# Performance work log

Hardware: AMD Instinct MI355X
Metric: run time of the kernel (lower is better)

The kernel has to match this reference:

```python
import jax, jax.numpy as jnp
import numpy as np
import math

EMBED_DIM = 1024
NUM_HEADS = 16
HEAD_DIM = EMBED_DIM // NUM_HEADS          # 64
SUB_HEAD_DIM = HEAD_DIM // 2               # 32
SCALING = 1.0 / math.sqrt(SUB_HEAD_DIM)
LAMBDA_INIT = 0.8 - 0.6 * math.exp(-0.3 * 0)  # layer_idx = 0 -> 0.2


def setup_inputs() -> dict:
    key = jax.random.key(0)
    ks = jax.random.split(key, 10)
    B, T, D = 2, 2048, EMBED_DIM
    xav = math.sqrt(6.0 / (D + D))  # xavier_uniform bound for square-ish mats
    return {
        "query": jax.random.normal(ks[0], (B, T, D), jnp.float32),
        "key": jax.random.normal(ks[1], (B, T, D), jnp.float32),
        "value": jax.random.normal(ks[2], (B, T, D), jnp.float32),
        "in_proj_weight": jax.random.uniform(ks[3], (3 * D, D), jnp.float32, -xav, xav),
        "in_proj_bias": jnp.zeros((3 * D,), jnp.float32),
        "out_proj_weight": jax.random.uniform(ks[4], (D, D), jnp.float32, -xav, xav),
        "out_proj_bias": jnp.zeros((D,), jnp.float32),
        "lambda_q1": 0.1 * jax.random.normal(ks[5], (SUB_HEAD_DIM,), jnp.float32),
        "lambda_k1": 0.1 * jax.random.normal(ks[6], (SUB_HEAD_DIM,), jnp.float32),
        "lambda_q2": 0.1 * jax.random.normal(ks[7], (SUB_HEAD_DIM,), jnp.float32),
        "lambda_k2": 0.1 * jax.random.normal(ks[8], (SUB_HEAD_DIM,), jnp.float32),
    }


def reference(query, key, value, in_proj_weight, in_proj_bias,
              out_proj_weight, out_proj_bias,
              lambda_q1, lambda_k1, lambda_q2, lambda_k2):
    B, T, D = query.shape
    S = key.shape[1]
    H, hd, sd = NUM_HEADS, HEAD_DIM, SUB_HEAD_DIM

    qw, kw, vw = jnp.split(in_proj_weight, 3, axis=0)
    qb, kb, vb = jnp.split(in_proj_bias, 3, axis=0)
    q = query @ qw.T + qb
    k = key @ kw.T + kb
    v = value @ vw.T + vb

    # [B, H, T, head_dim]
    q = q.reshape(B, T, H, hd).transpose(0, 2, 1, 3)
    k = k.reshape(B, S, H, hd).transpose(0, 2, 1, 3)
    v = v.reshape(B, S, H, hd).transpose(0, 2, 1, 3)

    q1, q2 = q[..., :sd], q[..., sd:]
    k1, k2 = k[..., :sd], k[..., sd:]

    logits_1 = jnp.einsum('bhtd,bhsd->bhts', q1, k1) * SCALING
    logits_2 = jnp.einsum('bhtd,bhsd->bhts', q2, k2) * SCALING

    a1 = jax.nn.softmax(logits_1, axis=-1)
    a2 = jax.nn.softmax(logits_2, axis=-1)

    lam = (jnp.exp(jnp.dot(lambda_q1, lambda_k1))
           - jnp.exp(jnp.dot(lambda_q2, lambda_k2)) + LAMBDA_INIT)

    diff_weights = a1 - lam * a2
    attn_output = jnp.einsum('bhts,bhsd->bhtd', diff_weights, v)
    attn_output = attn_output * (1.0 - LAMBDA_INIT)

    attn_output = attn_output.transpose(0, 2, 1, 3).reshape(B, T, D)
    output = attn_output @ out_proj_weight.T + out_proj_bias
    return output
```

## Files before the change

kernel.cpp:

```cpp
#include <hip/hip_runtime.h>
#include <cstdint>
#include <cstddef>

typedef unsigned short u16;
typedef __attribute__((ext_vector_type(8))) short bf16x8;
typedef __attribute__((ext_vector_type(4))) short bf16x4;
typedef __attribute__((ext_vector_type(4))) float f32x4;

__device__ __forceinline__ u16 f2bf(float f) {
  uint32_t u = __float_as_uint(f);
  u += 0x7fffu + ((u >> 16) & 1u);
  return (u16)(u >> 16);
}

__device__ __forceinline__ short f2bfs(float f) {
  __bf16 h = (__bf16)f;
  return __builtin_bit_cast(short, h);
}

__device__ __forceinline__ float bf2f(u16 u) {
  return __uint_as_float(((uint32_t)u) << 16);
}

#define MFMA16(a, b, c) __builtin_amdgcn_mfma_f32_16x16x32_bf16((a), (b), (c), 0, 0, 0)

__device__ __forceinline__ float ex2(float x) {
#if __has_builtin(__builtin_amdgcn_exp2f)
  return __builtin_amdgcn_exp2f(x);
#else
  return exp2f(x);
#endif
}

__global__ __launch_bounds__(256) void cvt_kernel(const float* __restrict__ in,
                                                  u16* __restrict__ out, int n8) {
  int i = blockIdx.x * blockDim.x + threadIdx.x;
  if (i >= n8) return;
  const float4* p = (const float4*)in;
  float4 a = p[i * 2], b = p[i * 2 + 1];
  u16 o[8] = {f2bf(a.x), f2bf(a.y), f2bf(a.z), f2bf(a.w),
              f2bf(b.x), f2bf(b.y), f2bf(b.z), f2bf(b.w)};
  *(int4*)(out + (size_t)i * 8) = *(const int4*)o;
}

template <typename OUT_T, bool SPLIT_A>
__global__ __launch_bounds__(256) void gemm_bt(const u16* __restrict__ Abase,
                                               const u16* __restrict__ B,
                                               const float* __restrict__ bias,
                                               OUT_T* __restrict__ C,
                                               u16* __restrict__ QH, u16* __restrict__ KH,
                                               u16* __restrict__ VT,
                                               int M, int N, int K) {
  __shared__ u16 As[128][40];
  __shared__ u16 Bs[128][40];
  const int nb = blockIdx.x, mb = blockIdx.y;
  const int t = threadIdx.x;
  const u16* A = Abase + (SPLIT_A ? (size_t)(nb >> 3) * (size_t)M * K : (size_t)0);
  const int w = t >> 6, lane = t & 63;
  const int wr = w >> 1, wc = w & 1;
  const int lr = lane & 15, lk = lane >> 4;
  const f32x4 zero4 = {0.f, 0.f, 0.f, 0.f};
  f32x4 acc[4][4];
#pragma unroll
  for (int i = 0; i < 4; ++i)
#pragma unroll
    for (int j = 0; j < 4; ++j) acc[i][j] = zero4;

  const int srow = t >> 2;
  const int scol = (t & 3) << 3;
  const u16* Ap = A + (size_t)(mb * 128 + srow) * K + scol;
  const u16* Bp = B + (size_t)(nb * 128 + srow) * K + scol;

  for (int k0 = 0; k0 < K; k0 += 32) {
    __syncthreads();
    *(int4*)&As[srow][scol]      = *(const int4*)(Ap + k0);
    *(int4*)&As[srow + 64][scol] = *(const int4*)(Ap + (size_t)64 * K + k0);
    *(int4*)&Bs[srow][scol]      = *(const int4*)(Bp + k0);
    *(int4*)&Bs[srow + 64][scol] = *(const int4*)(Bp + (size_t)64 * K + k0);
    __syncthreads();
    bf16x8 af[4], bfr[4];
#pragma unroll
    for (int mf = 0; mf < 4; ++mf) af[mf] = *(const bf16x8*)&As[wr * 64 + mf * 16 + lr][lk * 8];
#pragma unroll
    for (int nf = 0; nf < 4; ++nf) bfr[nf] = *(const bf16x8*)&Bs[wc * 64 + nf * 16 + lr][lk * 8];
#pragma unroll
    for (int mf = 0; mf < 4; ++mf)
#pragma unroll
      for (int nf = 0; nf < 4; ++nf) acc[mf][nf] = MFMA16(af[mf], bfr[nf], acc[mf][nf]);
  }

  if constexpr (SPLIT_A) {
    const int third = nb >> 3;
    const int bb = mb >> 4;
#pragma unroll
    for (int nf = 0; nf < 4; ++nf) {
      const int col = nb * 128 + wc * 64 + nf * 16 + lr;
      const int c = col & 1023;
      const int h = c >> 6, d = c & 63;
      const float bv = bias[col];
      u16* qk = (third == 0 ? QH : KH) + (size_t)(bb * 16 + h) * 2048 * 64;
      u16* vt = VT + ((size_t)(bb * 16 + h) * 64 + d) * 2048;
#pragma unroll
      for (int mf = 0; mf < 4; ++mf) {
        const int row0 = mb * 128 + wr * 64 + mf * 16 + lk * 4;
        const int s0 = row0 & 2047;
        if (third < 2) {
#pragma unroll
          for (int r = 0; r < 4; ++r)
            qk[(size_t)(s0 + r) * 64 + d] = f2bf(acc[mf][nf][r] + bv);
        } else {
          u16 tmp[4];
#pragma unroll
          for (int r = 0; r < 4; ++r) tmp[r] = f2bf(acc[mf][nf][r] + bv);
          *(uint2*)&vt[s0] = *(const uint2*)tmp;
        }
      }
    }
  } else {
#pragma unroll
    for (int nf = 0; nf < 4; ++nf) {
      const int col = nb * 128 + wc * 64 + nf * 16 + lr;
      const float bv = bias[col];
#pragma unroll
      for (int mf = 0; mf < 4; ++mf) {
        const int row0 = mb * 128 + wr * 64 + mf * 16 + lk * 4;
#pragma unroll
        for (int r = 0; r < 4; ++r)
          ((float*)C)[(size_t)(row0 + r) * N + col] = acc[mf][nf][r] + bv;
      }
    }
  }
}

__global__ __launch_bounds__(256, 4) void diff_attn(const u16* __restrict__ QH,
                                                    const u16* __restrict__ KH,
                                                    const u16* __restrict__ VT,
                                                    const float* __restrict__ lq1,
                                                    const float* __restrict__ lk1,
                                                    const float* __restrict__ lq2,
                                                    const float* __restrict__ lk2,
                                                    u16* __restrict__ ATTN) {
  __shared__ u16 Ks[64][68];
  __shared__ u16 Vs[64][68];
  const int t = threadIdx.x;
  const int id = blockIdx.x;
  const int swz = (id & 7) * 128 + (id >> 3);
  const int qt = swz & 31, bh = swz >> 5;
  const int b = bh >> 4, h = bh & 15;
  const int w = t >> 6, lane = t & 63;
  const int lr = lane & 15, lk = lane >> 4;
  const float QSC = 0.17677669529663687f * 1.4426950408889634f;

  float dd1 = 0.f, dd2 = 0.f;
  for (int i = 0; i < 32; ++i) { dd1 += lq1[i] * lk1[i]; dd2 += lq2[i] * lk2[i]; }
  const float lam = __expf(dd1) - __expf(dd2) + 0.2f;

  const int srow = t >> 3;
  const int scol = (t & 7) << 3;
  const int krow = ((srow & 4) << 2) | ((srow & 24) >> 1) | (srow & 3);
  const u16* qh = QH + (size_t)(b * 16 + h) * 2048 * 64;
  const u16* kh = KH + (size_t)(b * 16 + h) * 2048 * 64;
  const u16* vt = VT + (size_t)(b * 16 + h) * 64 * 2048;

  bf16x8 qa[2];
#pragma unroll
  for (int hh = 0; hh < 2; ++hh) {
    bf16x8 q = *(const bf16x8*)(qh + (size_t)(qt * 64 + w * 16 + lr) * 64 + hh * 32 + lk * 8);
#pragma unroll
    for (int i = 0; i < 8; ++i) q[i] = f2bfs(bf2f((u16)q[i]) * QSC);
    qa[hh] = q;
  }

  const f32x4 zero4 = {0.f, 0.f, 0.f, 0.f};
  f32x4 O[2][4], Ol[2];
#pragma unroll
  for (int hh = 0; hh < 2; ++hh) {
    Ol[hh] = zero4;
#pragma unroll
    for (int df = 0; df < 4; ++df) O[hh][df] = zero4;
  }
  bf16x8 vone8;
#pragma unroll
  for (int i = 0; i < 8; ++i) vone8[i] = (short)0x3F80;

  const u16* kp0 = kh + (size_t)srow * 64 + scol;
  const u16* kp1 = kp0 + (size_t)32 * 64;
  const u16* vp0 = vt + (size_t)srow * 2048 + scol;
  const u16* vp1 = vp0 + (size_t)32 * 2048;

  int4 kA0 = *(const int4*)kp0;
  int4 kA1 = *(const int4*)kp1;
  int4 vA0 = *(const int4*)vp0;
  int4 vA1 = *(const int4*)vp1;
  int4 kB0, kB1, vB0, vB1;

  for (int it = 0; it < 32; ++it) {
    __syncthreads();
    *(int4*)&Ks[krow][scol]      = kA0;
    *(int4*)&Ks[krow + 32][scol] = kA1;
    *(int4*)&Vs[srow][scol]      = vA0;
    *(int4*)&Vs[srow + 32][scol] = vA1;
    if (it < 31) {
      const int s1 = (it + 1) * 64;
      kB0 = *(const int4*)(kp0 + (size_t)s1 * 64);
      kB1 = *(const int4*)(kp1 + (size_t)s1 * 64);
      vB0 = *(const int4*)(vp0 + s1);
      vB1 = *(const int4*)(vp1 + s1);
    }
    __syncthreads();

    bf16x8 pk8[2][2];
#pragma unroll
    for (int hh = 0; hh < 2; ++hh) {
      f32x4 St[4];
#pragma unroll
      for (int nf = 0; nf < 4; ++nf) {
        bf16x8 kb = *(const bf16x8*)&Ks[nf * 16 + lr][hh * 32 + lk * 8];
        St[nf] = MFMA16(kb, qa[hh], zero4);
      }
#pragma unroll
      for (int j = 0; j < 2; ++j) {
        bf16x8 p;
#pragma unroll
        for (int a = 0; a < 2; ++a)
#pragma unroll
          for (int r = 0; r < 4; ++r)
            p[a * 4 + r] = f2bfs(ex2(St[2 * j + a][r]));
        pk8[hh][j] = p;
      }
    }

    __builtin_amdgcn_s_setprio(1);
#pragma unroll
    for (int j = 0; j < 2; ++j) {
      const bf16x8 pa0 = pk8[0][j], pa1 = pk8[1][j];
#pragma unroll
      for (int df = 0; df < 4; ++df) {
        bf16x8 vb = *(const bf16x8*)&Vs[df * 16 + lr][j * 32 + lk * 8];
        O[0][df] = MFMA16(pa0, vb, O[0][df]);
        O[1][df] = MFMA16(pa1, vb, O[1][df]);
      }
      Ol[0] = MFMA16(pa0, vone8, Ol[0]);
      Ol[1] = MFMA16(pa1, vone8, Ol[1]);
    }
    __builtin_amdgcn_s_setprio(0);

    kA0 = kB0; kA1 = kB1; vA0 = vB0; vA1 = vB1;
  }

  float i1[4], i2[4];
#pragma unroll
  for (int r = 0; r < 4; ++r) {
    i1[r] = 1.f / Ol[0][r];
    i2[r] = 1.f / Ol[1][r];
  }
  const size_t qrow0 = (size_t)b * 2048 + (size_t)qt * 64;
#pragma unroll
  for (int df = 0; df < 4; ++df) {
    const int col = h * 64 + df * 16 + lr;
#pragma unroll
    for (int r = 0; r < 4; ++r) {
      const size_t row = qrow0 + w * 16 + lk * 4 + r;
      float v = 0.8f * (O[0][df][r] * i1[r] - lam * O[1][df][r] * i2[r]);
      ATTN[row * 1024 + col] = f2bf(v);
    }
  }
}

extern "C" void kernel_launch(void* const* d_in, const int* in_sizes, int n_in,
                              void* d_out, int out_size, void* d_ws, size_t ws_size,
                              hipStream_t stream) {
  (void)in_sizes; (void)n_in; (void)out_size; (void)ws_size;
  const float* query = (const float*)d_in[0];
  const float* key_  = (const float*)d_in[1];
  const float* value = (const float*)d_in[2];
  const float* ipw   = (const float*)d_in[3];
  const float* ipb   = (const float*)d_in[4];
  const float* opw   = (const float*)d_in[5];
  const float* opb   = (const float*)d_in[6];
  const float* lq1   = (const float*)d_in[7];
  const float* lk1   = (const float*)d_in[8];
  const float* lq2   = (const float*)d_in[9];
  const float* lk2   = (const float*)d_in[10];

  const int M = 4096, D = 1024;
  u16* X    = (u16*)d_ws;
  u16* Wqkv = X + (size_t)3 * M * D;
  u16* Wout = Wqkv + (size_t)3 * D * D;
  u16* QH   = Wout + (size_t)D * D;
  u16* KH   = QH + (size_t)M * D;
  u16* VT   = KH + (size_t)M * D;
  u16* ATTN = VT + (size_t)M * D;

  auto cvt = [&](const float* src, u16* dst, size_t n) {
    int n8 = (int)(n / 8);
    cvt_kernel<<<dim3((n8 + 255) / 256), dim3(256), 0, stream>>>(src, dst, n8);
  };
  cvt(query, X, (size_t)M * D);
  cvt(key_,  X + (size_t)M * D, (size_t)M * D);
  cvt(value, X + (size_t)2 * M * D, (size_t)M * D);
  cvt(ipw, Wqkv, (size_t)3 * D * D);
  cvt(opw, Wout, (size_t)D * D);

  gemm_bt<u16, true><<<dim3(24, 32), dim3(256), 0, stream>>>(
      X, Wqkv, ipb, (u16*)nullptr, QH, KH, VT, M, 3 * D, D);
  diff_attn<<<dim3(1024), dim3(256), 0, stream>>>(QH, KH, VT, lq1, lk1, lq2, lk2, ATTN);
  gemm_bt<float, false><<<dim3(8, 32), dim3(256), 0, stream>>>(
      ATTN, Wout, opb, (float*)d_out, nullptr, nullptr, nullptr, M, D, D);
}
```

Before: 159.6 us.

## Double KV tile per attention iteration and batch fp32-to-bf16 conversion launches

The attention kernel now stages 128 keys and values per loop iteration instead of 64, halving the number of block-wide barriers and prefetch rounds, and processes the tile in two 64-key sub-steps. Shared memory per block roughly doubles, which may reduce how many blocks fit per CU under the 4-block launch bound, and more registers are spent on prefetch buffers. The five separate conversion launches are also merged into two kernels using the grid y dimension, cutting launch overhead.

New measurement: 412.0 us. 2.58x slower.

```diff
diff --git a/kernel.cpp b/kernel.cpp
--- a/kernel.cpp
+++ b/kernel.cpp
@@ -32,15 +32,41 @@
 #endif
 }
 
-__global__ __launch_bounds__(256) void cvt_kernel(const float* __restrict__ in,
-                                                  u16* __restrict__ out, int n8) {
+__global__ __launch_bounds__(256) void cvt3_kernel(const float* __restrict__ q,
+                                                   const float* __restrict__ k,
+                                                   const float* __restrict__ v,
+                                                   u16* __restrict__ out, int n8) {
   int i = blockIdx.x * blockDim.x + threadIdx.x;
   if (i >= n8) return;
-  const float4* p = (const float4*)in;
+  const float* src = blockIdx.y == 0 ? q : (blockIdx.y == 1 ? k : v);
+  u16* dst = out + (size_t)blockIdx.y * n8 * 8;
+  const float4* p = (const float4*)src;
   float4 a = p[i * 2], b = p[i * 2 + 1];
   u16 o[8] = {f2bf(a.x), f2bf(a.y), f2bf(a.z), f2bf(a.w),
               f2bf(b.x), f2bf(b.y), f2bf(b.z), f2bf(b.w)};
-  *(int4*)(out + (size_t)i * 8) = *(const int4*)o;
+  *(int4*)(dst + (size_t)i * 8) = *(const int4*)o;
+}
+
+__global__ __launch_bounds__(256) void cvtw_kernel(const float* __restrict__ w0,
+                                                   const float* __restrict__ w1,
+                                                   u16* __restrict__ o0,
+                                                   u16* __restrict__ o1,
+                                                   int n8_0, int n8_1) {
+  int i = blockIdx.x * blockDim.x + threadIdx.x;
+  const float* src;
+  u16* dst;
+  if (blockIdx.y == 0) {
+    if (i >= n8_0) return;
+    src = w0; dst = o0;
+  } else {
+    if (i >= n8_1) return;
+    src = w1; dst = o1;
+  }
+  const float4* p = (const float4*)src;
+  float4 a = p[i * 2], b = p[i * 2 + 1];
+  u16 o[8] = {f2bf(a.x), f2bf(a.y), f2bf(a.z), f2bf(a.w),
+              f2bf(b.x), f2bf(b.y), f2bf(b.z), f2bf(b.w)};
+  *(int4*)(dst + (size_t)i * 8) = *(const int4*)o;
 }
 
 template <typename OUT_T, bool SPLIT_A>
@@ -140,8 +166,8 @@
                                                     const float* __restrict__ lq2,
                                                     const float* __restrict__ lk2,
                                                     u16* __restrict__ ATTN) {
-  __shared__ u16 Ks[64][68];
-  __shared__ u16 Vs[64][68];
+  __shared__ u16 Ks[128][68];
+  __shared__ u16 Vs[64][136];
   const int t = threadIdx.x;
   const int id = blockIdx.x;
   const int swz = (id & 7) * 128 + (id >> 3);
@@ -183,69 +209,79 @@
 #pragma unroll
   for (int i = 0; i < 8; ++i) vone8[i] = (short)0x3F80;
 
-  const u16* kp0 = kh + (size_t)srow * 64 + scol;
-  const u16* kp1 = kp0 + (size_t)32 * 64;
-  const u16* vp0 = vt + (size_t)srow * 2048 + scol;
-  const u16* vp1 = vp0 + (size_t)32 * 2048;
-
-  int4 kA0 = *(const int4*)kp0;
-  int4 kA1 = *(const int4*)kp1;
-  int4 vA0 = *(const int4*)vp0;
-  int4 vA1 = *(const int4*)vp1;
-  int4 kB0, kB1, vB0, vB1;
-
-  for (int it = 0; it < 32; ++it) {
+  const u16* kp = kh + (size_t)srow * 64 + scol;
+  const u16* vp = vt + (size_t)srow * 2048 + scol;
+
+  int4 kA[4], vA[4], kB[4], vB[4];
+#pragma unroll
+  for (int kk = 0; kk < 4; ++kk) kA[kk] = *(const int4*)(kp + (size_t)(kk * 32) * 64);
+  vA[0] = *(const int4*)vp;
+  vA[1] = *(const int4*)(vp + 64);
+  vA[2] = *(const int4*)(vp + (size_t)32 * 2048);
+  vA[3] = *(const int4*)(vp + (size_t)32 * 2048 + 64);
+
+  for (int it = 0; it < 16; ++it) {
     __syncthreads();
-    *(int4*)&Ks[krow][scol]      = kA0;
-    *(int4*)&Ks[krow + 32][scol] = kA1;
-    *(int4*)&Vs[srow][scol]      = vA0;
-    *(int4*)&Vs[srow + 32][scol] = vA1;
-    if (it < 31) {
-      const int s1 = (it + 1) * 64;
-      kB0 = *(const int4*)(kp0 + (size_t)s1 * 64);
-      kB1 = *(const int4*)(kp1 + (size_t)s1 * 64);
-      vB0 = *(const int4*)(vp0 + s1);
-      vB1 = *(const int4*)(vp1 + s1);
+#pragma unroll
+    for (int kk = 0; kk < 4; ++kk)
+      *(int4*)&Ks[kk * 32 + krow][scol] = kA[kk];
+    *(int4*)&Vs[srow][scol]            = vA[0];
+    *(int4*)&Vs[srow][64 + scol]       = vA[1];
+    *(int4*)&Vs[srow + 32][scol]       = vA[2];
+    *(int4*)&Vs[srow + 32][64 + scol]  = vA[3];
+    if (it < 15) {
+      const int s1 = (it + 1) * 128;
+#pragma unroll
+      for (int kk = 0; kk < 4; ++kk)
+        kB[kk] = *(const int4*)(kp + (size_t)(s1 + kk * 32) * 64);
+      vB[0] = *(const int4*)(vp + s1);
+      vB[1] = *(const int4*)(vp + s1 + 64);
+      vB[2] = *(const int4*)(vp + (size_t)32 * 2048 + s1);
+      vB[3] = *(const int4*)(vp + (size_t)32 * 2048 + s1 + 64);
     }
     __syncthreads();
 
-    bf16x8 pk8[2][2];
-#pragma unroll
-    for (int hh = 0; hh < 2; ++hh) {
-      f32x4 St[4];
-#pragma unroll
-      for (int nf = 0; nf < 4; ++nf) {
-        bf16x8 kb = *(const bf16x8*)&Ks[nf * 16 + lr][hh * 32 + lk * 8];
-        St[nf] = MFMA16(kb, qa[hh], zero4);
+#pragma unroll
+    for (int sub = 0; sub < 2; ++sub) {
+      bf16x8 pk8[2][2];
+#pragma unroll
+      for (int hh = 0; hh < 2; ++hh) {
+        f32x4 St[4];
+#pragma unroll
+        for (int nf = 0; nf < 4; ++nf) {
+          bf16x8 kb = *(const bf16x8*)&Ks[sub * 64 + nf * 16 + lr][hh * 32 + lk * 8];
+          St[nf] = MFMA16(kb, qa[hh], zero4);
+        }
+#pragma unroll
+        for (int j = 0; j < 2; ++j) {
+          bf16x8 p;
+#pragma unroll
+          for (int a = 0; a < 2; ++a)
+#pragma unroll
+            for (int r = 0; r < 4; ++r)
+              p[a * 4 + r] = f2bfs(ex2(St[2 * j + a][r]));
+          pk8[hh][j] = p;
+        }
       }
+
+      __builtin_amdgcn_s_setprio(1);
 #pragma unroll
       for (int j = 0; j < 2; ++j) {
-        bf16x8 p;
-#pragma unroll
-        for (int a = 0; a < 2; ++a)
-#pragma unroll
-          for (int r = 0; r < 4; ++r)
-            p[a * 4 + r] = f2bfs(ex2(St[2 * j + a][r]));
-        pk8[hh][j] = p;
+        const bf16x8 pa0 = pk8[0][j], pa1 = pk8[1][j];
+#pragma unroll
+        for (int df = 0; df < 4; ++df) {
+          bf16x8 vb = *(const bf16x8*)&Vs[df * 16 + lr][sub * 64 + j * 32 + lk * 8];
+          O[0][df] = MFMA16(pa0, vb, O[0][df]);
+          O[1][df] = MFMA16(pa1, vb, O[1][df]);
+        }
+        Ol[0] = MFMA16(pa0, vone8, Ol[0]);
+        Ol[1] = MFMA16(pa1, vone8, Ol[1]);
       }
-    }
-
-    __builtin_amdgcn_s_setprio(1);
-#pragma unroll
-    for (int j = 0; j < 2; ++j) {
-      const bf16x8 pa0 = pk8[0][j], pa1 = pk8[1][j];
-#pragma unroll
-      for (int df = 0; df < 4; ++df) {
-        bf16x8 vb = *(const bf16x8*)&Vs[df * 16 + lr][j * 32 + lk * 8];
-        O[0][df] = MFMA16(pa0, vb, O[0][df]);
-        O[1][df] = MFMA16(pa1, vb, O[1][df]);
-      }
-      Ol[0] = MFMA16(pa0, vone8, Ol[0]);
-      Ol[1] = MFMA16(pa1, vone8, Ol[1]);
-    }
-    __builtin_amdgcn_s_setprio(0);
-
-    kA0 = kB0; kA1 = kB1; vA0 = vB0; vA1 = vB1;
+      __builtin_amdgcn_s_setprio(0);
+    }
+
+#pragma unroll
+    for (int kk = 0; kk < 4; ++kk) { kA[kk] = kB[kk]; vA[kk] = vB[kk]; }
   }
 
   float i1[4], i2[4];
@@ -292,15 +328,17 @@
   u16* VT   = KH + (size_t)M * D;
   u16* ATTN = VT + (size_t)M * D;
 
-  auto cvt = [&](const float* src, u16* dst, size_t n) {
-    int n8 = (int)(n / 8);
-    cvt_kernel<<<dim3((n8 + 255) / 256), dim3(256), 0, stream>>>(src, dst, n8);
-  };
-  cvt(query, X, (size_t)M * D);
-  cvt(key_,  X + (size_t)M * D, (size_t)M * D);
-  cvt(value, X + (size_t)2 * M * D, (size_t)M * D);
-  cvt(ipw, Wqkv, (size_t)3 * D * D);
-  cvt(opw, Wout, (size_t)D * D);
+  {
+    int n8 = (int)((size_t)M * D / 8);
+    cvt3_kernel<<<dim3((n8 + 255) / 256, 3), dim3(256), 0, stream>>>(
+        query, key_, value, X, n8);
+  }
+  {
+    int n8_0 = (int)((size_t)3 * D * D / 8);
+    int n8_1 = (int)((size_t)D * D / 8);
+    cvtw_kernel<<<dim3((n8_0 + 255) / 256, 2), dim3(256), 0, stream>>>(
+        ipw, opw, Wqkv, Wout, n8_0, n8_1);
+  }
 
   gemm_bt<u16, true><<<dim3(24, 32), dim3(256), 0, stream>>>(
       X, Wqkv, ipb, (u16*)nullptr, QH, KH, VT, M, 3 * D, D);
```

## Merge conversion launches and double GEMM K-tile to 64

Applied to the files above, without the earlier changes.

Five fp32-to-bf16 conversion launches are merged into two kernels that use a 2D grid, cutting launch overhead. The GEMM K-step is doubled from 32 to 64 and the LDS tiles are widened with padding to 68, halving the number of barrier-separated load/compute iterations. This uses more LDS per block, which may lower occupancy, and the new padding changes the bank-conflict pattern.

After: 145.8 us. 8.6% less time.

```diff
diff --git a/kernel.cpp b/kernel.cpp
--- a/kernel.cpp
+++ b/kernel.cpp
@@ -32,15 +32,41 @@
 #endif
 }
 
-__global__ __launch_bounds__(256) void cvt_kernel(const float* __restrict__ in,
-                                                  u16* __restrict__ out, int n8) {
+__global__ __launch_bounds__(256) void cvt3_kernel(const float* __restrict__ q,
+                                                   const float* __restrict__ k,
+                                                   const float* __restrict__ v,
+                                                   u16* __restrict__ out, int n8) {
   int i = blockIdx.x * blockDim.x + threadIdx.x;
   if (i >= n8) return;
-  const float4* p = (const float4*)in;
+  const float* src = blockIdx.y == 0 ? q : (blockIdx.y == 1 ? k : v);
+  u16* dst = out + (size_t)blockIdx.y * n8 * 8;
+  const float4* p = (const float4*)src;
   float4 a = p[i * 2], b = p[i * 2 + 1];
   u16 o[8] = {f2bf(a.x), f2bf(a.y), f2bf(a.z), f2bf(a.w),
               f2bf(b.x), f2bf(b.y), f2bf(b.z), f2bf(b.w)};
-  *(int4*)(out + (size_t)i * 8) = *(const int4*)o;
+  *(int4*)(dst + (size_t)i * 8) = *(const int4*)o;
+}
+
+__global__ __launch_bounds__(256) void cvtw_kernel(const float* __restrict__ w0,
+                                                   const float* __restrict__ w1,
+                                                   u16* __restrict__ o0,
+                                                   u16* __restrict__ o1,
+                                                   int n8_0, int n8_1) {
+  int i = blockIdx.x * blockDim.x + threadIdx.x;
+  const float* src;
+  u16* dst;
+  if (blockIdx.y == 0) {
+    if (i >= n8_0) return;
+    src = w0; dst = o0;
+  } else {
+    if (i >= n8_1) return;
+    src = w1; dst = o1;
+  }
+  const float4* p = (const float4*)src;
+  float4 a = p[i * 2], b = p[i * 2 + 1];
+  u16 o[8] = {f2bf(a.x), f2bf(a.y), f2bf(a.z), f2bf(a.w),
+              f2bf(b.x), f2bf(b.y), f2bf(b.z), f2bf(b.w)};
+  *(int4*)(dst + (size_t)i * 8) = *(const int4*)o;
 }
 
 template <typename OUT_T, bool SPLIT_A>
@@ -51,8 +77,8 @@
                                                u16* __restrict__ QH, u16* __restrict__ KH,
                                                u16* __restrict__ VT,
                                                int M, int N, int K) {
-  __shared__ u16 As[128][40];
-  __shared__ u16 Bs[128][40];
+  __shared__ u16 As[128][68];
+  __shared__ u16 Bs[128][68];
   const int nb = blockIdx.x, mb = blockIdx.y;
   const int t = threadIdx.x;
   const u16* A = Abase + (SPLIT_A ? (size_t)(nb >> 3) * (size_t)M * K : (size_t)0);
@@ -66,27 +92,33 @@
 #pragma unroll
     for (int j = 0; j < 4; ++j) acc[i][j] = zero4;
 
-  const int srow = t >> 2;
-  const int scol = (t & 3) << 3;
+  const int srow = t >> 3;
+  const int scol = (t & 7) << 3;
   const u16* Ap = A + (size_t)(mb * 128 + srow) * K + scol;
   const u16* Bp = B + (size_t)(nb * 128 + srow) * K + scol;
 
-  for (int k0 = 0; k0 < K; k0 += 32) {
+  for (int k0 = 0; k0 < K; k0 += 64) {
     __syncthreads();
-    *(int4*)&As[srow][scol]      = *(const int4*)(Ap + k0);
-    *(int4*)&As[srow + 64][scol] = *(const int4*)(Ap + (size_t)64 * K + k0);
-    *(int4*)&Bs[srow][scol]      = *(const int4*)(Bp + k0);
-    *(int4*)&Bs[srow + 64][scol] = *(const int4*)(Bp + (size_t)64 * K + k0);
+#pragma unroll
+    for (int j = 0; j < 4; ++j) {
+      *(int4*)&As[srow + 32 * j][scol] = *(const int4*)(Ap + (size_t)(32 * j) * K + k0);
+      *(int4*)&Bs[srow + 32 * j][scol] = *(const int4*)(Bp + (size_t)(32 * j) * K + k0);
+    }
     __syncthreads();
-    bf16x8 af[4], bfr[4];
-#pragma unroll
-    for (int mf = 0; mf < 4; ++mf) af[mf] = *(const bf16x8*)&As[wr * 64 + mf * 16 + lr][lk * 8];
-#pragma unroll
-    for (int nf = 0; nf < 4; ++nf) bfr[nf] = *(const bf16x8*)&Bs[wc * 64 + nf * 16 + lr][lk * 8];
-#pragma unroll
-    for (int mf = 0; mf < 4; ++mf)
-#pragma unroll
-      for (int nf = 0; nf < 4; ++nf) acc[mf][nf] = MFMA16(af[mf], bfr[nf], acc[mf][nf]);
+#pragma unroll
+    for (int kk = 0; kk < 2; ++kk) {
+      bf16x8 af[4], bfr[4];
+#pragma unroll
+      for (int mf = 0; mf < 4; ++mf)
+        af[mf] = *(const bf16x8*)&As[wr * 64 + mf * 16 + lr][kk * 32 + lk * 8];
+#pragma unroll
+      for (int nf = 0; nf < 4; ++nf)
+        bfr[nf] = *(const bf16x8*)&Bs[wc * 64 + nf * 16 + lr][kk * 32 + lk * 8];
+#pragma unroll
+      for (int mf = 0; mf < 4; ++mf)
+#pragma unroll
+        for (int nf = 0; nf < 4; ++nf) acc[mf][nf] = MFMA16(af[mf], bfr[nf], acc[mf][nf]);
+    }
   }
 
   if constexpr (SPLIT_A) {
@@ -292,15 +324,17 @@
   u16* VT   = KH + (size_t)M * D;
   u16* ATTN = VT + (size_t)M * D;
 
-  auto cvt = [&](const float* src, u16* dst, size_t n) {
-    int n8 = (int)(n / 8);
-    cvt_kernel<<<dim3((n8 + 255) / 256), dim3(256), 0, stream>>>(src, dst, n8);
-  };
-  cvt(query, X, (size_t)M * D);
-  cvt(key_,  X + (size_t)M * D, (size_t)M * D);
-  cvt(value, X + (size_t)2 * M * D, (size_t)M * D);
-  cvt(ipw, Wqkv, (size_t)3 * D * D);
-  cvt(opw, Wout, (size_t)D * D);
+  {
+    int n8 = (int)((size_t)M * D / 8);
+    cvt3_kernel<<<dim3((n8 + 255) / 256, 3), dim3(256), 0, stream>>>(
+        query, key_, value, X, n8);
+  }
+  {
+    int n8_0 = (int)((size_t)3 * D * D / 8);
+    int n8_1 = (int)((size_t)D * D / 8);
+    cvtw_kernel<<<dim3((n8_0 + 255) / 256, 2), dim3(256), 0, stream>>>(
+        ipw, opw, Wqkv, Wout, n8_0, n8_1);
+  }
 
   gemm_bt<u16, true><<<dim3(24, 32), dim3(256), 0, stream>>>(
       X, Wqkv, ipb, (u16*)nullptr, QH, KH, VT, M, 3 * D, D);
```
